# Kernel tuning notes

Measured on AMD Instinct MI355X. Metric: run time of the kernel, lower is better.

## Reference

```python
import jax, jax.numpy as jnp
import numpy as np

N, T, F_IN, E, H, FW = 4096, 64, 8, 256, 512, 32
LN_EPS = 1e-5


def setup_inputs() -> dict:
    key = jax.random.key(0)
    ks = jax.random.split(key, 16)
    nrm = lambda k, s, sc=0.05: jax.random.normal(k, s, dtype=jnp.float32) * sc
    return {
        "x": nrm(ks[0], (N, T, F_IN), 1.0),
        "We": nrm(ks[1], (E, F_IN)), "be": nrm(ks[2], (E,)),
        "Wih0": nrm(ks[3], (4 * H, E)), "Whh0": nrm(ks[4], (4 * H, H)),
        "bih0": nrm(ks[5], (4 * H,)), "bhh0": nrm(ks[6], (4 * H,)),
        "Wih1": nrm(ks[7], (4 * H, H)), "Whh1": nrm(ks[8], (4 * H, H)),
        "bih1": nrm(ks[9], (4 * H,)), "bhh1": nrm(ks[10], (4 * H,)),
        "fc1_w": nrm(ks[11], (H, H)), "fc1_b": nrm(ks[12], (H,)),
        "ln_g": jnp.ones((H,), jnp.float32), "ln_b": jnp.zeros((H,), jnp.float32),
        "fc2_w": nrm(ks[13], (F_IN, H)), "fc2_b": nrm(ks[14], (F_IN,)),
    }


def _cell(x, h, c, Wih, Whh, bih, bhh):
    # PyTorch LSTM gate order: i, f, g, o
    g = x @ Wih.T + h @ Whh.T + (bih + bhh)
    i, f, gg, o = jnp.split(g, 4, axis=-1)
    c = jax.nn.sigmoid(f) * c + jax.nn.sigmoid(i) * jnp.tanh(gg)
    h = jax.nn.sigmoid(o) * jnp.tanh(c)
    return h, c


def _layer(xs, Wih, Whh, bih, bhh):
    # xs: (T, N, D) -> ys: (T, N, H), final (h, c)
    n = xs.shape[1]
    Hd = Whh.shape[1]
    h0 = jnp.zeros((n, Hd), xs.dtype)
    def step(carry, x_t):
        h, c = carry
        h, c = _cell(x_t, h, c, Wih, Whh, bih, bhh)
        return (h, c), h
    (h, c), ys = jax.lax.scan(step, (h0, h0), xs)
    return ys, h, c


def reference(x, We, be, Wih0, Whh0, bih0, bhh0, Wih1, Whh1, bih1, bhh1,
              fc1_w, fc1_b, ln_g, ln_b, fc2_w, fc2_b):
    x_enc = x[:, :-1, :]          # (N, T-1, F)
    x0 = x[:, -1, :]              # (N, F)

    # ---- encoder ----
    emb = x_enc @ We.T + be       # (N, T-1, E)
    xs = jnp.swapaxes(emb, 0, 1)  # (T-1, N, E)
    ys0, h0e, c0e = _layer(xs, Wih0, Whh0, bih0, bhh0)
    _, h1e, c1e = _layer(ys0, Wih1, Whh1, bih1, bhh1)

    # ---- decoder head: Linear -> LayerNorm -> ReLU -> Linear ----
    def fc(h):
        z = h @ fc1_w.T + fc1_b
        mu = z.mean(-1, keepdims=True)
        var = z.var(-1, keepdims=True)
        z = (z - mu) * jax.lax.rsqrt(var + LN_EPS) * ln_g + ln_b
        z = jax.nn.relu(z)
        return z @ fc2_w.T + fc2_b

    def dec_step(carry, _):
        xt, h0, c0, h1, c1 = carry
        e = xt @ We.T + be
        h0, c0 = _cell(e, h0, c0, Wih0, Whh0, bih0, bhh0)
        h1, c1 = _cell(h0, h1, c1, Wih1, Whh1, bih1, bhh1)
        y = fc(h1)
        return (y, h0, c0, h1, c1), y

    _, ys = jax.lax.scan(dec_step, (x0, h0e, c0e, h1e, c1e), None, length=FW)
    return jnp.swapaxes(ys, 0, 1)  # (N, FW, F)
```

## Files before the change

### kernel.cpp

```cpp
#include <hip/hip_runtime.h>
#include <math.h>

#define NB   4096
#define HID  512
#define G4H  2048
#define EDIM 256
#define FINP 8
#define TSTEPS 64
#define FWIN 32

typedef __bf16 bf16;
typedef bf16  bf16x8 __attribute__((ext_vector_type(8)));
typedef float f32x4  __attribute__((ext_vector_type(4)));

__device__ __forceinline__ float sigf(float x) { return 1.0f / (1.0f + __expf(-x)); }
__device__ __forceinline__ float tanhf_(float x) { return 2.0f * sigf(2.0f * x) - 1.0f; }

__device__ __forceinline__ void gload16(const void* g, void* l) {
    __builtin_amdgcn_global_load_lds((const __attribute__((address_space(1))) void*)g,
                                     (__attribute__((address_space(3))) void*)l, 16, 0, 0);
}

__device__ __forceinline__ void swz32(int& bx, int& by) {
    int nwg  = (int)(gridDim.x * gridDim.y);
    int orig = (int)(blockIdx.x + blockIdx.y * gridDim.x);
    int swz  = (orig & 7) * (nwg >> 3) + (orig >> 3);
    bx = swz & 31;
    by = swz >> 5;
}

__device__ __forceinline__ void gemm_acc(
    const bf16* __restrict__ A1, const bf16* __restrict__ W1,
    const bf16* __restrict__ A2, const bf16* __restrict__ W2, int npass,
    int m0, int n0, bf16 (&As)[2][4096], bf16 (&Ws)[2][4096], f32x4 (&acc)[4][4])
{
    const int tid  = threadIdx.x;
    const int lane = tid & 63;
    const int w    = tid >> 6;
    const int wr   = w >> 1, wc = w & 1;
    const int koct = lane >> 4;
    const int l16  = lane & 15;
    const int lin0 = tid, lin1 = tid + 256;
    const int ar0 = lin0 >> 2, ac0 = (lin0 & 3) * 8;
    const int ar1 = lin1 >> 2, ac1 = (lin1 & 3) * 8;
    const int NK = npass << 4;

    auto stage = [&](int s, int b) {
        const bf16* A = (s < 16) ? A1 : A2;
        const bf16* W = (s < 16) ? W1 : W2;
        const int k0 = (s & 15) << 5;
        gload16(A + (size_t)(m0 + ar0) * HID + k0 + ac0, &As[b][lin0 * 8]);
        gload16(A + (size_t)(m0 + ar1) * HID + k0 + ac1, &As[b][lin1 * 8]);
        gload16(W + (size_t)(n0 + ar0) * HID + k0 + ac0, &Ws[b][lin0 * 8]);
        gload16(W + (size_t)(n0 + ar1) * HID + k0 + ac1, &Ws[b][lin1 * 8]);
    };

    stage(0, 0);
    __syncthreads();
    int cur = 0;
    for (int s = 0; s < NK; ++s) {
        if (s + 1 < NK) stage(s + 1, cur ^ 1);
        bf16x8 af[4], bfr[4];
#pragma unroll
        for (int m = 0; m < 4; ++m)
            af[m] = *(const bf16x8*)&As[cur][(wr * 64 + m * 16 + l16) * 32 + koct * 8];
#pragma unroll
        for (int n = 0; n < 4; ++n)
            bfr[n] = *(const bf16x8*)&Ws[cur][(wc * 64 + n * 16 + l16) * 32 + koct * 8];
#pragma unroll
        for (int m = 0; m < 4; ++m)
#pragma unroll
            for (int n = 0; n < 4; ++n)
                acc[m][n] = __builtin_amdgcn_mfma_f32_16x16x32_bf16(af[m], bfr[n], acc[m][n], 0, 0, 0);
        __syncthreads();
        cur ^= 1;
    }
}

template<bool HASX>
__device__ __forceinline__ void lstm_epi(f32x4 (&acc)[4][4],
    const float* __restrict__ Wfc, const float* __restrict__ bias,
    const float* __restrict__ xA, int sx,
    float* __restrict__ cst, bf16* __restrict__ hdst, int m0, int n0)
{
    const int tid = threadIdx.x, lane = tid & 63, w = tid >> 6;
    const int wr = w >> 1, wc = w & 1, l16 = lane & 15, lq = lane >> 4;
    const int hu = (n0 >> 2) + wc * 16 + l16;
    const int jb = n0 + wc * 64 + l16;

    float bq[4];
    f32x4 wf0[4], wf1[4];
#pragma unroll
    for (int g = 0; g < 4; ++g) {
        bq[g] = bias[jb + g * 16];
        if constexpr (HASX) {
            const float* wrow = Wfc + (size_t)(jb + g * 16) * 8;
            wf0[g] = *(const f32x4*)wrow;
            wf1[g] = *(const f32x4*)(wrow + 4);
        }
    }
#pragma unroll
    for (int m = 0; m < 4; ++m) {
        const int rb = m0 + wr * 64 + m * 16 + lq * 4;
#pragma unroll
        for (int q = 0; q < 4; ++q) {
            const int r = rb + q;
            float d0 = 0.f, d1 = 0.f, d2 = 0.f, d3 = 0.f;
            if constexpr (HASX) {
                const float* xr = xA + (size_t)r * sx;
                f32x4 xv0 = *(const f32x4*)xr;
                f32x4 xv1 = *(const f32x4*)(xr + 4);
                f32x4 p0 = xv0 * wf0[0] + xv1 * wf1[0];
                f32x4 p1 = xv0 * wf0[1] + xv1 * wf1[1];
                f32x4 p2 = xv0 * wf0[2] + xv1 * wf1[2];
                f32x4 p3 = xv0 * wf0[3] + xv1 * wf1[3];
                d0 = p0[0] + p0[1] + p0[2] + p0[3];
                d1 = p1[0] + p1[1] + p1[2] + p1[3];
                d2 = p2[0] + p2[1] + p2[2] + p2[3];
                d3 = p3[0] + p3[1] + p3[2] + p3[3];
            }
            float gi = acc[m][0][q] + bq[0] + d0;
            float gf = acc[m][1][q] + bq[1] + d1;
            float gg = acc[m][2][q] + bq[2] + d2;
            float go = acc[m][3][q] + bq[3] + d3;
            float iv = sigf(gi), fv = sigf(gf), gv = tanhf_(gg), ov = sigf(go);
            size_t ci = (size_t)r * HID + hu;
            float cn = fv * cst[ci] + iv * gv;
            cst[ci] = cn;
            hdst[ci] = (bf16)(ov * tanhf_(cn));
        }
    }
}

template<int NPASS, bool HASX>
__global__ __launch_bounds__(256)
void lstm_step(const bf16* __restrict__ A1, const bf16* __restrict__ W1,
               const bf16* __restrict__ A2, const bf16* __restrict__ W2,
               const float* __restrict__ Wfc, const float* __restrict__ bias,
               const float* __restrict__ xA, int sx,
               float* __restrict__ cst, bf16* __restrict__ hdst)
{
    __shared__ bf16 As[2][4096], Ws[2][4096];
    int bx, by; swz32(bx, by);
    const int m0 = bx * 128, n0 = by * 128;
    f32x4 acc[4][4];
#pragma unroll
    for (int m = 0; m < 4; ++m)
#pragma unroll
        for (int n = 0; n < 4; ++n) acc[m][n] = (f32x4){0.f, 0.f, 0.f, 0.f};
    gemm_acc(A1, W1, A2, W2, NPASS, m0, n0, As, Ws, acc);
    lstm_epi<HASX>(acc, Wfc, bias, xA, sx, cst, hdst, m0, n0);
}

template<bool L1TWO>
__global__ __launch_bounds__(256)
void enc_fused(const bf16* __restrict__ h0_in, const bf16* __restrict__ Whh0c,
               const float* __restrict__ Wf0c, const float* __restrict__ bf0c,
               const float* __restrict__ xA,
               bf16* __restrict__ h0_out, float* __restrict__ c0,
               const bf16* __restrict__ Wih1c, const bf16* __restrict__ h1_in,
               const bf16* __restrict__ Whh1c, const float* __restrict__ bs1c,
               bf16* __restrict__ h1_out, float* __restrict__ c1)
{
    __shared__ bf16 As[2][4096], Ws[2][4096];
    int bx, by; swz32(bx, by);
    const int m0 = bx * 128;
    f32x4 acc[4][4];
#pragma unroll
    for (int m = 0; m < 4; ++m)
#pragma unroll
        for (int n = 0; n < 4; ++n) acc[m][n] = (f32x4){0.f, 0.f, 0.f, 0.f};
    if (by < 16) {
        const int n0 = by * 128;
        gemm_acc(h0_in, Whh0c, nullptr, nullptr, 1, m0, n0, As, Ws, acc);
        lstm_epi<true>(acc, Wf0c, bf0c, xA, TSTEPS * FINP, c0, h0_out, m0, n0);
    } else {
        const int n0 = (by - 16) * 128;
        gemm_acc(h0_in, Wih1c, h1_in, Whh1c, L1TWO ? 2 : 1, m0, n0, As, Ws, acc);
        lstm_epi<false>(acc, nullptr, bs1c, nullptr, 0, c1, h1_out, m0, n0);
    }
}

__global__ __launch_bounds__(256)
void init_step(const float* __restrict__ x, const float* __restrict__ Wf0c,
               const float* __restrict__ bf0c, bf16* __restrict__ h0,
               float* __restrict__ c0)
{
    int idx = blockIdx.x * 256 + threadIdx.x;
    int r = idx >> 9, hu = idx & 511;
    const float* xr = x + (size_t)r * (TSTEPS * FINP);
    f32x4 xv0 = *(const f32x4*)xr;
    f32x4 xv1 = *(const f32x4*)(xr + 4);
    int jb = ((hu >> 4) << 6) + (hu & 15);
    float g[4];
#pragma unroll
    for (int gg = 0; gg < 4; ++gg) {
        const float* wrow = Wf0c + (size_t)(jb + gg * 16) * 8;
        f32x4 w0 = *(const f32x4*)wrow;
        f32x4 w1 = *(const f32x4*)(wrow + 4);
        f32x4 p = xv0 * w0 + xv1 * w1;
        g[gg] = bf0c[jb + gg * 16] + p[0] + p[1] + p[2] + p[3];
    }
    float iv = sigf(g[0]), gv = tanhf_(g[2]), ov = sigf(g[3]);
    float cn = iv * gv;
    c0[idx] = cn;
    h0[idx] = (bf16)(ov * tanhf_(cn));
}

__global__ __launch_bounds__(256)
void fc1_mfma(const bf16* __restrict__ A, const bf16* __restrict__ W,
              const float* __restrict__ bias, float* __restrict__ Z)
{
    __shared__ bf16 As[2][4096], Ws[2][4096];
    int bx, by; swz32(bx, by);
    const int m0 = bx * 128, n0 = by * 128;
    f32x4 acc[4][4];
#pragma unroll
    for (int m = 0; m < 4; ++m)
#pragma unroll
        for (int n = 0; n < 4; ++n) acc[m][n] = (f32x4){0.f, 0.f, 0.f, 0.f};
    gemm_acc(A, W, nullptr, nullptr, 1, m0, n0, As, Ws, acc);

    const int tid = threadIdx.x, lane = tid & 63, w = tid >> 6;
    const int wr = w >> 1, wc = w & 1, l16 = lane & 15, lq = lane >> 4;
#pragma unroll
    for (int m = 0; m < 4; ++m) {
        const int rb = m0 + wr * 64 + m * 16 + lq * 4;
#pragma unroll
        for (int n = 0; n < 4; ++n) {
            const int col = n0 + wc * 64 + n * 16 + l16;
            float bv = bias[col];
#pragma unroll
            for (int q = 0; q < 4; ++q)
                Z[(size_t)(rb + q) * HID + col] = acc[m][n][q] + bv;
        }
    }
}

__global__ __launch_bounds__(256)
void ln_fc2_kernel(const float* __restrict__ Z, const float* __restrict__ lng,
                   const float* __restrict__ lnb, const float* __restrict__ w2,
                   const float* __restrict__ b2, float* __restrict__ out)
{
    int wave = threadIdx.x >> 6;
    int lane = threadIdx.x & 63;
    int n = blockIdx.x * 4 + wave;
    const float* zr = Z + (size_t)n * HID;

    float v[8];
    float s1 = 0.f, s2 = 0.f;
#pragma unroll
    for (int j = 0; j < 8; ++j) {
        v[j] = zr[lane + j * 64];
        s1 += v[j];
        s2 += v[j] * v[j];
    }
#pragma unroll
    for (int off = 32; off; off >>= 1) {
        s1 += __shfl_down(s1, off);
        s2 += __shfl_down(s2, off);
    }
    s1 = __shfl(s1, 0);
    s2 = __shfl(s2, 0);
    float mu = s1 * (1.f / 512.f);
    float var = s2 * (1.f / 512.f) - mu * mu;
    float rs = rsqrtf(var + 1e-5f);

    float y[8];
#pragma unroll
    for (int f = 0; f < 8; ++f) y[f] = 0.f;
#pragma unroll
    for (int j = 0; j < 8; ++j) {
        int h = lane + j * 64;
        float zn = (v[j] - mu) * rs * lng[h] + lnb[h];
        zn = fmaxf(zn, 0.f);
#pragma unroll
        for (int f = 0; f < 8; ++f) y[f] += zn * w2[f * HID + h];
    }
#pragma unroll
    for (int f = 0; f < 8; ++f)
#pragma unroll
        for (int off = 32; off; off >>= 1) y[f] += __shfl_down(y[f], off);

    if (lane == 0) {
#pragma unroll
        for (int f = 0; f < 8; ++f) out[(size_t)n * 256 + f] = y[f] + b2[f];
    }
}

__device__ __forceinline__ int remap_j(int j) {
    int gate = j >> 9, hu = j & 511;
    return ((hu >> 4) << 6) + (gate << 4) + (hu & 15);
}

__global__ void fold_small(const float* __restrict__ Wih0, const float* __restrict__ We,
                           const float* __restrict__ be, const float* __restrict__ bih0,
                           const float* __restrict__ bhh0, const float* __restrict__ bih1,
                           const float* __restrict__ bhh1,
                           float* __restrict__ Wf0c, float* __restrict__ bf0c,
                           float* __restrict__ bs1c)
{
    int j = blockIdx.x * 256 + threadIdx.x;
    if (j >= G4H) return;
    int jn = remap_j(j);
    float acc[FINP];
#pragma unroll
    for (int f = 0; f < FINP; ++f) acc[f] = 0.f;
    float bacc = 0.f;
    for (int e = 0; e < EDIM; ++e) {
        float wv = Wih0[(size_t)j * EDIM + e];
        bacc += wv * be[e];
#pragma unroll
        for (int f = 0; f < FINP; ++f) acc[f] += wv * We[e * FINP + f];
    }
#pragma unroll
    for (int f = 0; f < FINP; ++f) Wf0c[(size_t)jn * FINP + f] = acc[f];
    bf0c[jn] = bacc + bih0[j] + bhh0[j];
    bs1c[jn] = bih1[j] + bhh1[j];
}

__global__ void conv_w(const float* __restrict__ W0, const float* __restrict__ W1,
                       const float* __restrict__ W2,
                       bf16* __restrict__ O0, bf16* __restrict__ O1, bf16* __restrict__ O2)
{
    int j = blockIdx.x;
    int which = blockIdx.y;
    const float* src = which == 0 ? W0 : which == 1 ? W1 : W2;
    bf16* dst = which == 0 ? O0 : which == 1 ? O1 : O2;
    int jn = remap_j(j);
    for (int k = threadIdx.x; k < HID; k += 256)
        dst[(size_t)jn * HID + k] = (bf16)src[(size_t)j * HID + k];
}

__global__ void conv_fc1(const float* __restrict__ W, bf16* __restrict__ O)
{
    int j = blockIdx.x;
    for (int k = threadIdx.x; k < HID; k += 256)
        O[(size_t)j * HID + k] = (bf16)W[(size_t)j * HID + k];
}

extern "C" void kernel_launch(void* const* d_in, const int* in_sizes, int n_in,
                              void* d_out, int out_size, void* d_ws, size_t ws_size,
                              hipStream_t stream)
{
    const float* x    = (const float*)d_in[0];
    const float* We   = (const float*)d_in[1];
    const float* be   = (const float*)d_in[2];
    const float* Wih0 = (const float*)d_in[3];
    const float* Whh0 = (const float*)d_in[4];
    const float* bih0 = (const float*)d_in[5];
    const float* bhh0 = (const float*)d_in[6];
    const float* Wih1 = (const float*)d_in[7];
    const float* Whh1 = (const float*)d_in[8];
    const float* bih1 = (const float*)d_in[9];
    const float* bhh1 = (const float*)d_in[10];
    const float* fc1w = (const float*)d_in[11];
    const float* fc1b = (const float*)d_in[12];
    const float* lng  = (const float*)d_in[13];
    const float* lnb  = (const float*)d_in[14];
    const float* fc2w = (const float*)d_in[15];
    const float* fc2b = (const float*)d_in[16];
    float* out = (float*)d_out;

    char* p = (char*)d_ws;
    auto alloc = [&](size_t bytes) -> void* {
        void* r = (void*)p;
        p += (bytes + 255) & ~(size_t)255;
        return r;
    };
    bf16*  Whh0c = (bf16*)alloc((size_t)G4H * HID * 2);
    bf16*  Wih1c = (bf16*)alloc((size_t)G4H * HID * 2);
    bf16*  Whh1c = (bf16*)alloc((size_t)G4H * HID * 2);
    bf16*  fc1wb = (bf16*)alloc((size_t)HID * HID * 2);
    float* Wf0c  = (float*)alloc((size_t)G4H * FINP * 4);
    float* bf0c  = (float*)alloc((size_t)G4H * 4);
    float* bs1c  = (float*)alloc((size_t)G4H * 4);
    const size_t S = (size_t)NB * HID;
    bf16*  H0[2]; H0[0] = (bf16*)alloc(S * 2); H0[1] = (bf16*)alloc(S * 2);
    bf16*  H1[2]; H1[0] = (bf16*)alloc(S * 2); H1[1] = (bf16*)alloc(S * 2);
    float* c0    = (float*)alloc(S * 4);
    float* c1    = (float*)alloc(S * 4);
    float* Z     = (float*)alloc(S * 4);

    hipMemsetAsync(c1, 0, S * 4, stream);

    fold_small<<<8, 256, 0, stream>>>(Wih0, We, be, bih0, bhh0, bih1, bhh1, Wf0c, bf0c, bs1c);
    conv_w<<<dim3(G4H, 3), 256, 0, stream>>>(Whh0, Wih1, Whh1, Whh0c, Wih1c, Whh1c);
    conv_fc1<<<HID, 256, 0, stream>>>(fc1w, fc1wb);

    init_step<<<NB * HID / 256, 256, 0, stream>>>(x, Wf0c, bf0c, H0[0], c0);

    dim3 fg(32, 32), lb(256);
    for (int t = 0; t < TSTEPS - 2; ++t) {
        if (t == 0)
            enc_fused<false><<<fg, lb, 0, stream>>>(H0[0], Whh0c, Wf0c, bf0c,
                x + (size_t)1 * FINP, H0[1], c0,
                Wih1c, nullptr, Whh1c, bs1c, H1[0], c1);
        else
            enc_fused<true><<<fg, lb, 0, stream>>>(H0[t & 1], Whh0c, Wf0c, bf0c,
                x + (size_t)(t + 1) * FINP, H0[(t + 1) & 1], c0,
                Wih1c, H1[(t + 1) & 1], Whh1c, bs1c, H1[t & 1], c1);
    }
    lstm_step<2, false><<<dim3(32, 16), lb, 0, stream>>>(
        H0[0], Wih1c, H1[1], Whh1c, nullptr, bs1c, nullptr, 0, c1, H1[0]);

    for (int s = 0; s < FWIN; ++s) {
        const float* xA = (s == 0) ? (x + (size_t)(TSTEPS - 1) * FINP)
                                   : (out + (size_t)(s - 1) * FINP);
        int sx = (s == 0) ? (TSTEPS * FINP) : (FWIN * FINP);
        lstm_step<1, true><<<dim3(32, 16), lb, 0, stream>>>(
            H0[s & 1], Whh0c, nullptr, nullptr, Wf0c, bf0c, xA, sx, c0, H0[(s + 1) & 1]);
        lstm_step<2, false><<<dim3(32, 16), lb, 0, stream>>>(
            H0[(s + 1) & 1], Wih1c, H1[s & 1], Whh1c, nullptr, bs1c, nullptr, 0,
            c1, H1[(s + 1) & 1]);
        fc1_mfma<<<dim3(32, 4), lb, 0, stream>>>(H1[(s + 1) & 1], fc1wb, fc1b, Z);
        ln_fc2_kernel<<<NB / 4, 256, 0, stream>>>(Z, lng, lnb, fc2w, fc2b,
                                                  out + (size_t)s * FINP);
    }
}
```

Before: 6.196 ms.

## Store GEMM tiles in MFMA fragment order and use explicit vmcnt waits

The shared-memory tile layout is changed so each wave's 64 lanes read one contiguous 512-element fragment block. This replaces the strided row-by-32 reads, which likely caused LDS bank conflicts. The __syncthreads calls are replaced with raw s_barrier plus explicit s_waitcnt vmcnt counts, so the next stage's global-to-LDS loads can stay in flight while the current tile is consumed. This relies on hand-counted outstanding loads (vmcnt(4)) being correct, which is a correctness risk if the compiler reorders or adds memory ops.

Result: slower. 8.353 ms (+34.8%).

```diff
diff --git a/kernel.cpp b/kernel.cpp
--- a/kernel.cpp
+++ b/kernel.cpp
@@ -38,41 +38,49 @@
     const int lane = tid & 63;
     const int w    = tid >> 6;
     const int wr   = w >> 1, wc = w & 1;
-    const int koct = lane >> 4;
-    const int l16  = lane & 15;
-    const int lin0 = tid, lin1 = tid + 256;
-    const int ar0 = lin0 >> 2, ac0 = (lin0 & 3) * 8;
-    const int ar1 = lin1 >> 2, ac1 = (lin1 & 3) * 8;
-    const int NK = npass << 4;
+    const int NK   = npass << 4;
+
+    const int r0 = ((tid >> 6) << 4) + (tid & 15);
+    const int o0 = ((tid >> 4) & 3) * 8;
+    const int t1 = tid + 256;
+    const int r1 = ((t1 >> 6) << 4) + (t1 & 15);
+    const int o1 = ((t1 >> 4) & 3) * 8;
 
     auto stage = [&](int s, int b) {
         const bf16* A = (s < 16) ? A1 : A2;
         const bf16* W = (s < 16) ? W1 : W2;
         const int k0 = (s & 15) << 5;
-        gload16(A + (size_t)(m0 + ar0) * HID + k0 + ac0, &As[b][lin0 * 8]);
-        gload16(A + (size_t)(m0 + ar1) * HID + k0 + ac1, &As[b][lin1 * 8]);
-        gload16(W + (size_t)(n0 + ar0) * HID + k0 + ac0, &Ws[b][lin0 * 8]);
-        gload16(W + (size_t)(n0 + ar1) * HID + k0 + ac1, &Ws[b][lin1 * 8]);
+        gload16(A + (size_t)(m0 + r0) * HID + k0 + o0, &As[b][tid * 8]);
+        gload16(A + (size_t)(m0 + r1) * HID + k0 + o1, &As[b][(tid + 256) * 8]);
+        gload16(W + (size_t)(n0 + r0) * HID + k0 + o0, &Ws[b][tid * 8]);
+        gload16(W + (size_t)(n0 + r1) * HID + k0 + o1, &Ws[b][(tid + 256) * 8]);
     };
 
     stage(0, 0);
-    __syncthreads();
+    asm volatile("s_waitcnt vmcnt(0)" ::: "memory");
+    __builtin_amdgcn_s_barrier();
     int cur = 0;
     for (int s = 0; s < NK; ++s) {
-        if (s + 1 < NK) stage(s + 1, cur ^ 1);
+        if (s + 1 < NK) {
+            stage(s + 1, cur ^ 1);
+            asm volatile("s_waitcnt vmcnt(4)" ::: "memory");
+        } else {
+            asm volatile("s_waitcnt vmcnt(0)" ::: "memory");
+        }
+        __builtin_amdgcn_s_barrier();
+        const bf16* abase = &As[cur][(wr << 2) * 512 + lane * 8];
+        const bf16* bbase = &Ws[cur][(wc << 2) * 512 + lane * 8];
         bf16x8 af[4], bfr[4];
 #pragma unroll
-        for (int m = 0; m < 4; ++m)
-            af[m] = *(const bf16x8*)&As[cur][(wr * 64 + m * 16 + l16) * 32 + koct * 8];
-#pragma unroll
-        for (int n = 0; n < 4; ++n)
-            bfr[n] = *(const bf16x8*)&Ws[cur][(wc * 64 + n * 16 + l16) * 32 + koct * 8];
+        for (int m = 0; m < 4; ++m) af[m] = *(const bf16x8*)(abase + m * 512);
+#pragma unroll
+        for (int n = 0; n < 4; ++n) bfr[n] = *(const bf16x8*)(bbase + n * 512);
 #pragma unroll
         for (int m = 0; m < 4; ++m)
 #pragma unroll
             for (int n = 0; n < 4; ++n)
                 acc[m][n] = __builtin_amdgcn_mfma_f32_16x16x32_bf16(af[m], bfr[n], acc[m][n], 0, 0, 0);
-        __syncthreads();
+        __builtin_amdgcn_s_barrier();
         cur ^= 1;
     }
 }
@@ -140,7 +148,7 @@
                const float* __restrict__ xA, int sx,
                float* __restrict__ cst, bf16* __restrict__ hdst)
 {
-    __shared__ bf16 As[2][4096], Ws[2][4096];
+    __shared__ __align__(16) bf16 As[2][4096], Ws[2][4096];
     int bx, by; swz32(bx, by);
     const int m0 = bx * 128, n0 = by * 128;
     f32x4 acc[4][4];
@@ -162,7 +170,7 @@
                const bf16* __restrict__ Whh1c, const float* __restrict__ bs1c,
                bf16* __restrict__ h1_out, float* __restrict__ c1)
 {
-    __shared__ bf16 As[2][4096], Ws[2][4096];
+    __shared__ __align__(16) bf16 As[2][4096], Ws[2][4096];
     int bx, by; swz32(bx, by);
     const int m0 = bx * 128;
     f32x4 acc[4][4];
@@ -211,7 +219,7 @@
 void fc1_mfma(const bf16* __restrict__ A, const bf16* __restrict__ W,
               const float* __restrict__ bias, float* __restrict__ Z)
 {
-    __shared__ bf16 As[2][4096], Ws[2][4096];
+    __shared__ __align__(16) bf16 As[2][4096], Ws[2][4096];
     int bx, by; swz32(bx, by);
     const int m0 = bx * 128, n0 = by * 128;
     f32x4 acc[4][4];
```
